# Performance work log

Hardware: AMD Instinct MI355X
Metric: run time of the kernel (lower is better)

The kernel has to match this reference:

```python
import jax, jax.numpy as jnp
import numpy as np

NUM_GROUPS = 32
EPS = 1e-6

def group_norm(x, gamma, beta):
    b, c, h, w = x.shape
    xg = x.reshape(b, NUM_GROUPS, c // NUM_GROUPS, h, w)
    mean = xg.mean(axis=(2, 3, 4), keepdims=True)
    var = xg.var(axis=(2, 3, 4), keepdims=True)
    xg = (xg - mean) * jax.lax.rsqrt(var + EPS)
    x = xg.reshape(b, c, h, w)
    return x * gamma[None, :, None, None] + beta[None, :, None, None]

def conv1x1(x, w, b):
    # x: [B,C,H,W], w: [Cout,Cin], b: [Cout]
    return jnp.einsum('bchw,oc->bohw', x, w) + b[None, :, None, None]

def setup_inputs() -> dict:
    key = jax.random.key(0)
    ks = jax.random.split(key, 11)
    B, C, H, W = 4, 512, 64, 64
    s = 1.0 / np.sqrt(C)
    return {
        'x': jax.random.normal(ks[0], (B, C, H, W), dtype=jnp.float32),
        'gn_gamma': jnp.ones((C,), jnp.float32),
        'gn_beta': jnp.zeros((C,), jnp.float32),
        'wq': jax.random.normal(ks[1], (C, C), jnp.float32) * s,
        'bq': jnp.zeros((C,), jnp.float32),
        'wk': jax.random.normal(ks[2], (C, C), jnp.float32) * s,
        'bk': jnp.zeros((C,), jnp.float32),
        'wv': jax.random.normal(ks[3], (C, C), jnp.float32) * s,
        'bv': jnp.zeros((C,), jnp.float32),
        'wo': jax.random.normal(ks[4], (C, C), jnp.float32) * s,
        'bo': jnp.zeros((C,), jnp.float32),
    }

def reference(x, gn_gamma, gn_beta, wq, bq, wk, bk, wv, bv, wo, bo):
    b, c, H, W = x.shape
    h = group_norm(x, gn_gamma, gn_beta)
    q = conv1x1(h, wq, bq).reshape(b, c, H * W).transpose(0, 2, 1)  # [B, HW, C]
    k = conv1x1(h, wk, bk).reshape(b, c, H * W)                      # [B, C, HW]
    v = conv1x1(h, wv, bv).reshape(b, c, H * W).transpose(0, 2, 1)  # [B, HW, C]
    attn = jnp.einsum('bnc,bcm->bnm', q, k) * (c ** -0.5)            # [B, HW, HW]
    attn = jax.nn.softmax(attn, axis=-1)
    out = jnp.einsum('bnm,bmc->bnc', attn, v)                        # [B, HW, C]
    out = out.transpose(0, 2, 1).reshape(b, c, H, W)
    return x + conv1x1(out, wo, bo)
```

## Files before the change

### kernel.cpp

```cpp
#include <hip/hip_runtime.h>
#include <cstdint>
#include <cstddef>

typedef __attribute__((ext_vector_type(8))) short short8;
typedef __attribute__((ext_vector_type(8))) _Float16 half8;
typedef __attribute__((ext_vector_type(4))) float f32x4;
typedef __attribute__((ext_vector_type(16))) float f32x16;

#define C_ 512
#define S_ 4096
#define B_ 4
#define EPS_ 1e-6f
#define SCALE_ 0.04419417382415922f

__device__ __forceinline__ ushort f2bf(float f) {
    union { float f; uint32_t u; } v; v.f = f;
    uint32_t r = v.u + 0x7FFFu + ((v.u >> 16) & 1u);
    return (ushort)(r >> 16);
}

__global__ void wconv_kernel(const float* __restrict__ wq, const float* __restrict__ wk,
                             const float* __restrict__ wv, const float* __restrict__ wo,
                             ushort* __restrict__ out) {
    int i = blockIdx.x * 256 + threadIdx.x;
    out[i]          = f2bf(wq[i]);
    out[262144 + i] = f2bf(wk[i]);
    out[524288 + i] = f2bf(wv[i]);
    out[786432 + i] = f2bf(wo[i]);
}

__global__ __launch_bounds__(512) void gn_stats_kernel(const float* __restrict__ x,
                                                       float* __restrict__ stats) {
    int bg = blockIdx.x;
    const float* xp = x + (size_t)bg * 16 * S_;
    float sum = 0.f, ss = 0.f;
    for (int i = threadIdx.x; i < 16 * S_; i += 512) {
        float v = xp[i];
        sum += v; ss += v * v;
    }
    #pragma unroll
    for (int off = 32; off; off >>= 1) {
        sum += __shfl_down(sum, off);
        ss  += __shfl_down(ss, off);
    }
    __shared__ float r0[8], r1[8];
    int wid = threadIdx.x >> 6;
    if ((threadIdx.x & 63) == 0) { r0[wid] = sum; r1[wid] = ss; }
    __syncthreads();
    if (threadIdx.x == 0) {
        float ts = 0.f, tq = 0.f;
        #pragma unroll
        for (int w = 0; w < 8; w++) { ts += r0[w]; tq += r1[w]; }
        float mean = ts / 65536.f;
        float var  = tq / 65536.f - mean * mean;
        stats[bg * 2]     = mean;
        stats[bg * 2 + 1] = rsqrtf(var + EPS_);
    }
}

__global__ __launch_bounds__(256) void gn_apply_kernel(const float* __restrict__ x,
        const float* __restrict__ gamma, const float* __restrict__ beta,
        const float* __restrict__ stats, ushort* __restrict__ h_t) {
    int sc = blockIdx.x, g = blockIdx.y, b = blockIdx.z;
    int c0 = g * 16;
    int bg = b * 32 + g;
    float mean = stats[bg * 2], rstd = stats[bg * 2 + 1];
    int t = threadIdx.x;
    __shared__ float tile[16][257];
    const float* xp = x + ((size_t)b * C_ + c0) * S_ + sc * 256;
    {
        int c = t >> 4, s0 = (t & 15) * 4;
        const float* src = xp + (size_t)c * S_;
        #pragma unroll
        for (int j = 0; j < 4; j++) {
            float4 d = *(const float4*)(src + s0 + 64 * j);
            tile[c][s0 + 64 * j + 0] = d.x;
            tile[c][s0 + 64 * j + 1] = d.y;
            tile[c][s0 + 64 * j + 2] = d.z;
            tile[c][s0 + 64 * j + 3] = d.w;
        }
    }
    __syncthreads();
    {
        float vv[16];
        #pragma unroll
        for (int ci = 0; ci < 16; ci++) {
            float a = rstd * gamma[c0 + ci];
            float bb2 = beta[c0 + ci] - mean * a;
            vv[ci] = tile[ci][t] * a + bb2;
        }
        uint4 lo, hi;
        lo.x = (uint32_t)f2bf(vv[0])  | ((uint32_t)f2bf(vv[1])  << 16);
        lo.y = (uint32_t)f2bf(vv[2])  | ((uint32_t)f2bf(vv[3])  << 16);
        lo.z = (uint32_t)f2bf(vv[4])  | ((uint32_t)f2bf(vv[5])  << 16);
        lo.w = (uint32_t)f2bf(vv[6])  | ((uint32_t)f2bf(vv[7])  << 16);
        hi.x = (uint32_t)f2bf(vv[8])  | ((uint32_t)f2bf(vv[9])  << 16);
        hi.y = (uint32_t)f2bf(vv[10]) | ((uint32_t)f2bf(vv[11]) << 16);
        hi.z = (uint32_t)f2bf(vv[12]) | ((uint32_t)f2bf(vv[13]) << 16);
        hi.w = (uint32_t)f2bf(vv[14]) | ((uint32_t)f2bf(vv[15]) << 16);
        ushort* dst = h_t + ((size_t)b * S_ + sc * 256 + t) * C_ + c0;
        *(uint4*)dst = lo;
        *(uint4*)(dst + 8) = hi;
    }
}

template <int MODE>
__global__ __launch_bounds__(256, 2) void gemm_kernel(
        const ushort* __restrict__ A,
        const ushort* __restrict__ Bt,
        const float* __restrict__ bias,
        void* __restrict__ outp,
        const float* __restrict__ xres,
        float scale) {
    int bb = blockIdx.z;
    int m0 = blockIdx.y * 64;
    int n0 = blockIdx.x * 128;
    const ushort* Bp = Bt + (size_t)bb * S_ * C_ + (size_t)n0 * C_;
    __shared__ ushort Al[64 * 64];
    __shared__ ushort Bl[128 * 64];
    int t = threadIdx.x, lane = t & 63, wid = t >> 6;
    int wm = (wid >> 1) * 32, wn = (wid & 1) * 64;
    f32x4 acc[2][4] = {};
    for (int k0 = 0; k0 < 512; k0 += 64) {
        #pragma unroll
        for (int i = 0; i < 2; i++) {
            int cid = t + i * 256;
            int row = cid >> 3, cc = cid & 7;
            uint4 d = *(const uint4*)(A + (size_t)(m0 + row) * 512 + k0 + cc * 8);
            *(uint4*)((char*)Al + row * 128 + ((cc * 16) ^ ((row & 7) << 4))) = d;
        }
        #pragma unroll
        for (int i = 0; i < 4; i++) {
            int cid = t + i * 256;
            int row = cid >> 3, cc = cid & 7;
            uint4 d = *(const uint4*)(Bp + (size_t)row * 512 + k0 + cc * 8);
            *(uint4*)((char*)Bl + row * 128 + ((cc * 16) ^ ((row & 7) << 4))) = d;
        }
        __syncthreads();
        #pragma unroll
        for (int ks = 0; ks < 2; ks++) {
            short8 af[2], bfrag[4];
            #pragma unroll
            for (int i = 0; i < 2; i++) {
                int row = wm + i * 16 + (lane & 15);
                af[i] = *(const short8*)((char*)Al + row * 128 + ((ks * 64 + (lane >> 4) * 16) ^ ((row & 7) << 4)));
            }
            #pragma unroll
            for (int j = 0; j < 4; j++) {
                int row = wn + j * 16 + (lane & 15);
                bfrag[j] = *(const short8*)((char*)Bl + row * 128 + ((ks * 64 + (lane >> 4) * 16) ^ ((row & 7) << 4)));
            }
            #pragma unroll
            for (int i = 0; i < 2; i++)
                #pragma unroll
                for (int j = 0; j < 4; j++)
                    acc[i][j] = __builtin_amdgcn_mfma_f32_16x16x32_bf16(af[i], bfrag[j], acc[i][j], 0, 0, 0);
        }
        __syncthreads();
    }
    int rr = (lane >> 4) * 4;
    #pragma unroll
    for (int i = 0; i < 2; i++) {
        int mb = m0 + wm + i * 16 + rr;
        float bs[4];
        #pragma unroll
        for (int r = 0; r < 4; r++) bs[r] = bias[mb + r];
        #pragma unroll
        for (int j = 0; j < 4; j++) {
            int n = n0 + wn + j * 16 + (lane & 15);
            if (MODE == 0) {
                ushort* O = (ushort*)outp + (size_t)bb * S_ * C_ + (size_t)n * C_ + mb;
                uint2 pp;
                pp.x = (uint32_t)f2bf((acc[i][j][0] + bs[0]) * scale) |
                       ((uint32_t)f2bf((acc[i][j][1] + bs[1]) * scale) << 16);
                pp.y = (uint32_t)f2bf((acc[i][j][2] + bs[2]) * scale) |
                       ((uint32_t)f2bf((acc[i][j][3] + bs[3]) * scale) << 16);
                *(uint2*)O = pp;
            } else if (MODE == 1) {
                ushort* O = (ushort*)outp + (size_t)bb * C_ * S_ + (size_t)mb * S_ + n;
                #pragma unroll
                for (int r = 0; r < 4; r++) O[(size_t)r * S_] = f2bf(acc[i][j][r] + bs[r]);
            } else {
                float* O = (float*)outp + (size_t)bb * C_ * S_ + (size_t)mb * S_ + n;
                const float* X = xres + (size_t)bb * C_ * S_ + (size_t)mb * S_ + n;
                #pragma unroll
                for (int r = 0; r < 4; r++) O[(size_t)r * S_] = X[(size_t)r * S_] + acc[i][j][r] + bs[r];
            }
        }
    }
}

#define KBUF_SZ  65536
#define SLDS_OFF 131072
#define PLDS_OFF 149504
#define STM_OFF  158720

__device__ __forceinline__ void stage_k(const ushort* kp, int kv0, int wid, int lane, char* Kbuf) {
    #pragma unroll
    for (int p = 0; p < 8; p++) {
        int row = wid * 8 + p;
        const char* src = (const char*)(kp + (size_t)(kv0 + row) * C_) + ((lane * 16) ^ ((row & 7) << 4));
        __builtin_amdgcn_global_load_lds(
            (const __attribute__((address_space(1))) unsigned int*)src,
            (__attribute__((address_space(3))) unsigned int*)(Kbuf + row * 1024),
            16, 0, 0);
    }
}

__global__ __launch_bounds__(512, 2) void attn_kernel(const ushort* __restrict__ q_t,
        const ushort* __restrict__ k_t, const ushort* __restrict__ v,
        ushort* __restrict__ ao_t) {
    constexpr int NIT = S_ / 64;
    int qb = blockIdx.x, bb = blockIdx.y;
    int s0 = qb * 64;
    const ushort* qp = q_t + (size_t)bb * S_ * C_;
    const ushort* kp = k_t + (size_t)bb * S_ * C_;
    const ushort* vp = v   + (size_t)bb * C_ * S_;

    extern __shared__ char lds[];
    char* Kbuf0 = lds;
    char* Kbuf1 = lds + KBUF_SZ;
    _Float16* S_lds = (_Float16*)(lds + SLDS_OFF);
    char*  P_lds = lds + PLDS_OFF;
    float* st_m  = (float*)(lds + STM_OFF);
    float* st_l  = st_m + 64;
    float* st_f  = st_m + 128;

    int t = threadIdx.x, lane = t & 63, wid = t >> 6;
    int l31 = lane & 31, lh = lane >> 5;
    int qt = (wid >> 2) & 1, nt = (wid >> 1) & 1, ch = wid & 1;

    if (t < 64) { st_m[t] = -1e30f; st_l[t] = 0.f; }

    short8 qf[16];
    {
        const ushort* qrow = qp + (size_t)(s0 + qt * 32 + l31) * C_ + ch * 256 + lh * 8;
        #pragma unroll
        for (int ks = 0; ks < 16; ks++)
            qf[ks] = *(const short8*)(qrow + ks * 16);
    }
    f32x16 o_[2][2] = {};

    stage_k(kp, 0, wid, lane, Kbuf0);
    asm volatile("s_waitcnt vmcnt(0) lgkmcnt(0)" ::: "memory");
    __builtin_amdgcn_s_barrier();
    asm volatile("" ::: "memory");

    for (int it = 0; it < NIT; it++) {
        int kv0 = it * 64;
        char* Kcur = (it & 1) ? Kbuf1 : Kbuf0;
        char* Knxt = (it & 1) ? Kbuf0 : Kbuf1;

        short8 vb[2][4];
        {
            const ushort* vdb = vp + (size_t)(wid * 64 + l31) * S_ + kv0 + lh * 8;
            #pragma unroll
            for (int dt = 0; dt < 2; dt++)
                #pragma unroll
                for (int ks2 = 0; ks2 < 4; ks2++)
                    vb[dt][ks2] = *(const short8*)(vdb + (size_t)dt * 32 * S_ + ks2 * 16);
        }
        if (it + 1 < NIT)
            stage_k(kp, kv0 + 64, wid, lane, Knxt);

        f32x16 sacc = {};
        {
            int krow = nt * 32 + l31;
            const char* kb = Kcur + krow * 1024;
            int sw = (krow & 7) << 4;
            int cb0 = ch * 512 + lh * 16;
            #pragma unroll
            for (int ks = 0; ks < 16; ks++) {
                short8 kf = *(const short8*)(kb + ((cb0 + ks * 32) ^ sw));
                sacc = __builtin_amdgcn_mfma_f32_32x32x16_bf16(qf[ks], kf, sacc, 0, 0, 0);
            }
        }
        {
            _Float16* Sp = S_lds + (size_t)ch * 4608 + (size_t)(qt * 32) * 72 + nt * 32 + l31;
            #pragma unroll
            for (int r = 0; r < 16; r++) {
                int qrow = (r & 3) + 8 * (r >> 2) + 4 * lh;
                Sp[qrow * 72] = (_Float16)sacc[r];
            }
        }
        asm volatile("s_waitcnt lgkmcnt(0)" ::: "memory");
        __builtin_amdgcn_s_barrier();
        asm volatile("" ::: "memory");

        {
            int row = t >> 3, j = t & 7;
            half8 h0 = *(const half8*)((const char*)S_lds + (size_t)row * 144 + j * 16);
            half8 h1 = *(const half8*)((const char*)S_lds + 9216 + (size_t)row * 144 + j * 16);
            float sv[8];
            #pragma unroll
            for (int i = 0; i < 8; i++) sv[i] = (float)h0[i] + (float)h1[i];
            float mx = sv[0];
            #pragma unroll
            for (int i = 1; i < 8; i++) mx = fmaxf(mx, sv[i]);
            mx = fmaxf(mx, __shfl_xor(mx, 1));
            mx = fmaxf(mx, __shfl_xor(mx, 2));
            mx = fmaxf(mx, __shfl_xor(mx, 4));
            float mold = st_m[row];
            float mnew = fmaxf(mold, mx);
            float ps = 0.f;
            uint32_t pk[4];
            #pragma unroll
            for (int i = 0; i < 4; i++) {
                float p0 = __expf(sv[2 * i]     - mnew);
                float p1 = __expf(sv[2 * i + 1] - mnew);
                ps += p0 + p1;
                pk[i] = (uint32_t)f2bf(p0) | ((uint32_t)f2bf(p1) << 16);
            }
            *(uint4*)(P_lds + (size_t)row * 144 + j * 16) = *(uint4*)pk;
            ps += __shfl_xor(ps, 1); ps += __shfl_xor(ps, 2); ps += __shfl_xor(ps, 4);
            float f = __expf(mold - mnew);
            if (j == 0) {
                st_m[row] = mnew;
                st_l[row] = st_l[row] * f + ps;
                st_f[row] = f;
            }
        }
        asm volatile("s_waitcnt lgkmcnt(0)" ::: "memory");
        __builtin_amdgcn_s_barrier();
        asm volatile("" ::: "memory");

        {
            #pragma unroll
            for (int qt2 = 0; qt2 < 2; qt2++) {
                f32x4 f0 = *(const f32x4*)(st_f + qt2 * 32 + 0  + 4 * lh);
                f32x4 f1 = *(const f32x4*)(st_f + qt2 * 32 + 8  + 4 * lh);
                f32x4 f2 = *(const f32x4*)(st_f + qt2 * 32 + 16 + 4 * lh);
                f32x4 f3 = *(const f32x4*)(st_f + qt2 * 32 + 24 + 4 * lh);
                float fr[16];
                #pragma unroll
                for (int e = 0; e < 4; e++) {
                    fr[e] = f0[e]; fr[4 + e] = f1[e]; fr[8 + e] = f2[e]; fr[12 + e] = f3[e];
                }
                #pragma unroll
                for (int dt = 0; dt < 2; dt++)
                    #pragma unroll
                    for (int r = 0; r < 16; r++)
                        o_[qt2][dt][r] *= fr[r];
            }
            short8 pa[2][4];
            #pragma unroll
            for (int qt2 = 0; qt2 < 2; qt2++)
                #pragma unroll
                for (int ks2 = 0; ks2 < 4; ks2++)
                    pa[qt2][ks2] = *(const short8*)(P_lds + (size_t)(qt2 * 32 + l31) * 144 + ks2 * 32 + lh * 16);
            #pragma unroll
            for (int qt2 = 0; qt2 < 2; qt2++)
                #pragma unroll
                for (int dt = 0; dt < 2; dt++)
                    #pragma unroll
                    for (int ks2 = 0; ks2 < 4; ks2++)
                        o_[qt2][dt] = __builtin_amdgcn_mfma_f32_32x32x16_bf16(pa[qt2][ks2], vb[dt][ks2], o_[qt2][dt], 0, 0, 0);
        }
        asm volatile("s_waitcnt vmcnt(0) lgkmcnt(0)" ::: "memory");
        __builtin_amdgcn_s_barrier();
        asm volatile("" ::: "memory");
    }

    #pragma unroll
    for (int qt2 = 0; qt2 < 2; qt2++) {
        f32x4 l0 = *(const f32x4*)(st_l + qt2 * 32 + 0  + 4 * lh);
        f32x4 l1 = *(const f32x4*)(st_l + qt2 * 32 + 8  + 4 * lh);
        f32x4 l2 = *(const f32x4*)(st_l + qt2 * 32 + 16 + 4 * lh);
        f32x4 l3 = *(const f32x4*)(st_l + qt2 * 32 + 24 + 4 * lh);
        float rl[16];
        #pragma unroll
        for (int e = 0; e < 4; e++) {
            rl[e] = 1.0f / l0[e]; rl[4 + e] = 1.0f / l1[e];
            rl[8 + e] = 1.0f / l2[e]; rl[12 + e] = 1.0f / l3[e];
        }
        #pragma unroll
        for (int dt = 0; dt < 2; dt++) {
            int d = wid * 64 + dt * 32 + l31;
            #pragma unroll
            for (int r = 0; r < 16; r++) {
                int q = qt2 * 32 + (r & 3) + 8 * (r >> 2) + 4 * lh;
                ao_t[((size_t)bb * S_ + s0 + q) * C_ + d] = f2bf(o_[qt2][dt][r] * rl[r]);
            }
        }
    }
}

extern "C" void kernel_launch(void* const* d_in, const int* in_sizes, int n_in,
                              void* d_out, int out_size, void* d_ws, size_t ws_size,
                              hipStream_t stream) {
    const float* x  = (const float*)d_in[0];
    const float* gg = (const float*)d_in[1];
    const float* gb = (const float*)d_in[2];
    const float* wq = (const float*)d_in[3];
    const float* bq = (const float*)d_in[4];
    const float* wk = (const float*)d_in[5];
    const float* bk = (const float*)d_in[6];
    const float* wv = (const float*)d_in[7];
    const float* bv = (const float*)d_in[8];
    const float* wo = (const float*)d_in[9];
    const float* bo = (const float*)d_in[10];
    float* out = (float*)d_out;

    char* ws = (char*)d_ws;
    const size_t BUF = (size_t)B_ * S_ * C_ * 2;
    ushort* h_t  = (ushort*)(ws);
    ushort* q_t  = (ushort*)(ws + BUF);
    ushort* k_t  = (ushort*)(ws + 2 * BUF);
    ushort* v_n  = (ushort*)(ws + 3 * BUF);
    ushort* ao_t = (ushort*)(ws + 4 * BUF);
    ushort* wb   = (ushort*)(ws + 5 * BUF);
    float* stats = (float*)(ws + 5 * BUF + 4 * 524288);

    wconv_kernel<<<1024, 256, 0, stream>>>(wq, wk, wv, wo, wb);
    gn_stats_kernel<<<128, 512, 0, stream>>>(x, stats);
    gn_apply_kernel<<<dim3(16, 32, B_), 256, 0, stream>>>(x, gg, gb, stats, h_t);

    dim3 ggrid(32, 8, B_);
    gemm_kernel<0><<<ggrid, 256, 0, stream>>>(wb,          h_t, bq, (void*)q_t, nullptr, SCALE_);
    gemm_kernel<0><<<ggrid, 256, 0, stream>>>(wb + 262144, h_t, bk, (void*)k_t, nullptr, 1.0f);
    gemm_kernel<1><<<ggrid, 256, 0, stream>>>(wb + 524288, h_t, bv, (void*)v_n, nullptr, 1.0f);

    attn_kernel<<<dim3(64, B_), 512, 159488, stream>>>(q_t, k_t, v_n, ao_t);

    gemm_kernel<2><<<ggrid, 256, 0, stream>>>(wb + 786432, ao_t, bo, (void*)out, x, 1.0f);
}
```

Before: 467.4 us.

## Enlarge GEMM tiles with async LDS double-buffering and lazy softmax rescale in attention

The projection GEMM moves to 128x128 tiles using 32x32x16 MFMA, with double-buffered LDS filled by global_load_lds, so one barrier per k-step overlaps loads with compute. The attention kernel remaps block IDs to a 1D grid that interleaves batches and query blocks, and hoists the V base pointer. It also adds a lazy online-softmax rescale: the running max is updated only when it grows by more than a threshold, and a shared flag skips the output rescale multiply otherwise. The lazy rescale assumes exponent headroom and adds an extra LDS flag with its reset.

```diff
diff --git a/kernel.cpp b/kernel.cpp
--- a/kernel.cpp
+++ b/kernel.cpp
@@ -113,78 +113,104 @@
         const float* __restrict__ xres,
         float scale) {
     int bb = blockIdx.z;
-    int m0 = blockIdx.y * 64;
+    int m0 = blockIdx.y * 128;
     int n0 = blockIdx.x * 128;
-    const ushort* Bp = Bt + (size_t)bb * S_ * C_ + (size_t)n0 * C_;
-    __shared__ ushort Al[64 * 64];
-    __shared__ ushort Bl[128 * 64];
+    const ushort* Ap = A + (size_t)m0 * 512;
+    const ushort* Bp = Bt + (size_t)bb * S_ * C_ + (size_t)n0 * 512;
+
+    extern __shared__ char lds[];
+
     int t = threadIdx.x, lane = t & 63, wid = t >> 6;
-    int wm = (wid >> 1) * 32, wn = (wid & 1) * 64;
-    f32x4 acc[2][4] = {};
+    int l31 = lane & 31, lh = lane >> 5;
+    int wm = (wid >> 1) * 64, wn = (wid & 1) * 64;
+
+    f32x16 acc[2][2] = {};
+
+    #define G_STAGE(sbuf, k0)                                                            \
+        {                                                                                \
+            char* Adst = lds + (sbuf) * 16384;                                           \
+            char* Bdst = lds + 32768 + (sbuf) * 16384;                                   \
+            _Pragma("unroll")                                                            \
+            for (int i_ = 0; i_ < 4; i_++) {                                             \
+                int cb = wid * 64 + i_ * 256;                                            \
+                int cid = cb + lane;                                                     \
+                int row = cid >> 3, c16 = cid & 7;                                       \
+                int sw = ((c16 * 16) ^ ((row & 7) << 4));                                \
+                const char* sa = (const char*)(Ap + (size_t)row * 512 + (k0)) + sw;      \
+                __builtin_amdgcn_global_load_lds(                                        \
+                    (const __attribute__((address_space(1))) unsigned int*)sa,           \
+                    (__attribute__((address_space(3))) unsigned int*)(Adst + cb * 16),   \
+                    16, 0, 0);                                                           \
+                const char* sb = (const char*)(Bp + (size_t)row * 512 + (k0)) + sw;      \
+                __builtin_amdgcn_global_load_lds(                                        \
+                    (const __attribute__((address_space(1))) unsigned int*)sb,           \
+                    (__attribute__((address_space(3))) unsigned int*)(Bdst + cb * 16),   \
+                    16, 0, 0);                                                           \
+            }                                                                            \
+        }
+
+    G_STAGE(0, 0);
+    asm volatile("s_waitcnt vmcnt(0)" ::: "memory");
+    __builtin_amdgcn_s_barrier();
+    asm volatile("" ::: "memory");
+
     for (int k0 = 0; k0 < 512; k0 += 64) {
-        #pragma unroll
-        for (int i = 0; i < 2; i++) {
-            int cid = t + i * 256;
-            int row = cid >> 3, cc = cid & 7;
-            uint4 d = *(const uint4*)(A + (size_t)(m0 + row) * 512 + k0 + cc * 8);
-            *(uint4*)((char*)Al + row * 128 + ((cc * 16) ^ ((row & 7) << 4))) = d;
-        }
-        #pragma unroll
-        for (int i = 0; i < 4; i++) {
-            int cid = t + i * 256;
-            int row = cid >> 3, cc = cid & 7;
-            uint4 d = *(const uint4*)(Bp + (size_t)row * 512 + k0 + cc * 8);
-            *(uint4*)((char*)Bl + row * 128 + ((cc * 16) ^ ((row & 7) << 4))) = d;
-        }
-        __syncthreads();
-        #pragma unroll
-        for (int ks = 0; ks < 2; ks++) {
-            short8 af[2], bfrag[4];
+        int s = (k0 >> 6) & 1;
+        if (k0 + 64 < 512) G_STAGE(s ^ 1, k0 + 64);
+        char* Al = lds + s * 16384;
+        char* Bl = lds + 32768 + s * 16384;
+        #pragma unroll
+        for (int ks = 0; ks < 4; ks++) {
+            short8 af[2], bfr[2];
             #pragma unroll
             for (int i = 0; i < 2; i++) {
-                int row = wm + i * 16 + (lane & 15);
-                af[i] = *(const short8*)((char*)Al + row * 128 + ((ks * 64 + (lane >> 4) * 16) ^ ((row & 7) << 4)));
-            }
-            #pragma unroll
-            for (int j = 0; j < 4; j++) {
-                int row = wn + j * 16 + (lane & 15);
-                bfrag[j] = *(const short8*)((char*)Bl + row * 128 + ((ks * 64 + (lane >> 4) * 16) ^ ((row & 7) << 4)));
+                int rowa = wm + i * 32 + l31;
+                af[i] = *(const short8*)(Al + rowa * 128 + ((ks * 32 + lh * 16) ^ ((rowa & 7) << 4)));
+                int rowb = wn + i * 32 + l31;
+                bfr[i] = *(const short8*)(Bl + rowb * 128 + ((ks * 32 + lh * 16) ^ ((rowb & 7) << 4)));
             }
             #pragma unroll
             for (int i = 0; i < 2; i++)
                 #pragma unroll
-                for (int j = 0; j < 4; j++)
-                    acc[i][j] = __builtin_amdgcn_mfma_f32_16x16x32_bf16(af[i], bfrag[j], acc[i][j], 0, 0, 0);
-        }
-        __syncthreads();
-    }
-    int rr = (lane >> 4) * 4;
+                for (int j = 0; j < 2; j++)
+                    acc[i][j] = __builtin_amdgcn_mfma_f32_32x32x16_bf16(af[i], bfr[j], acc[i][j], 0, 0, 0);
+        }
+        asm volatile("s_waitcnt vmcnt(0) lgkmcnt(0)" ::: "memory");
+        __builtin_amdgcn_s_barrier();
+        asm volatile("" ::: "memory");
+    }
+    #undef G_STAGE
+
     #pragma unroll
     for (int i = 0; i < 2; i++) {
-        int mb = m0 + wm + i * 16 + rr;
-        float bs[4];
-        #pragma unroll
-        for (int r = 0; r < 4; r++) bs[r] = bias[mb + r];
-        #pragma unroll
-        for (int j = 0; j < 4; j++) {
-            int n = n0 + wn + j * 16 + (lane & 15);
-            if (MODE == 0) {
-                ushort* O = (ushort*)outp + (size_t)bb * S_ * C_ + (size_t)n * C_ + mb;
-                uint2 pp;
-                pp.x = (uint32_t)f2bf((acc[i][j][0] + bs[0]) * scale) |
-                       ((uint32_t)f2bf((acc[i][j][1] + bs[1]) * scale) << 16);
-                pp.y = (uint32_t)f2bf((acc[i][j][2] + bs[2]) * scale) |
-                       ((uint32_t)f2bf((acc[i][j][3] + bs[3]) * scale) << 16);
-                *(uint2*)O = pp;
-            } else if (MODE == 1) {
-                ushort* O = (ushort*)outp + (size_t)bb * C_ * S_ + (size_t)mb * S_ + n;
-                #pragma unroll
-                for (int r = 0; r < 4; r++) O[(size_t)r * S_] = f2bf(acc[i][j][r] + bs[r]);
-            } else {
-                float* O = (float*)outp + (size_t)bb * C_ * S_ + (size_t)mb * S_ + n;
-                const float* X = xres + (size_t)bb * C_ * S_ + (size_t)mb * S_ + n;
-                #pragma unroll
-                for (int r = 0; r < 4; r++) O[(size_t)r * S_] = X[(size_t)r * S_] + acc[i][j][r] + bs[r];
+        #pragma unroll
+        for (int q = 0; q < 4; q++) {
+            int mbase = m0 + wm + i * 32 + q * 8 + 4 * lh;
+            float bs[4];
+            #pragma unroll
+            for (int r = 0; r < 4; r++) bs[r] = bias[mbase + r];
+            #pragma unroll
+            for (int j = 0; j < 2; j++) {
+                int n = n0 + wn + j * 32 + l31;
+                if (MODE == 0) {
+                    ushort* O = (ushort*)outp + ((size_t)bb * S_ + n) * C_ + mbase;
+                    uint2 pp;
+                    pp.x = (uint32_t)f2bf((acc[i][j][q * 4 + 0] + bs[0]) * scale) |
+                           ((uint32_t)f2bf((acc[i][j][q * 4 + 1] + bs[1]) * scale) << 16);
+                    pp.y = (uint32_t)f2bf((acc[i][j][q * 4 + 2] + bs[2]) * scale) |
+                           ((uint32_t)f2bf((acc[i][j][q * 4 + 3] + bs[3]) * scale) << 16);
+                    *(uint2*)O = pp;
+                } else if (MODE == 1) {
+                    ushort* O = (ushort*)outp + (size_t)bb * C_ * S_ + (size_t)mbase * S_ + n;
+                    #pragma unroll
+                    for (int r = 0; r < 4; r++) O[(size_t)r * S_] = f2bf(acc[i][j][q * 4 + r] + bs[r]);
+                } else {
+                    float* O = (float*)outp + (size_t)bb * C_ * S_ + (size_t)mbase * S_ + n;
+                    const float* X = xres + (size_t)bb * C_ * S_ + (size_t)mbase * S_ + n;
+                    #pragma unroll
+                    for (int r = 0; r < 4; r++)
+                        O[(size_t)r * S_] = X[(size_t)r * S_] + acc[i][j][q * 4 + r] + bs[r];
+                }
             }
         }
     }
@@ -211,7 +237,9 @@
         const ushort* __restrict__ k_t, const ushort* __restrict__ v,
         ushort* __restrict__ ao_t) {
     constexpr int NIT = S_ / 64;
-    int qb = blockIdx.x, bb = blockIdx.y;
+    int id = blockIdx.x;
+    int bb = (id & 7) >> 1;
+    int qb = ((id & 1) << 5) | (id >> 3);
     int s0 = qb * 64;
     const ushort* qp = q_t + (size_t)bb * S_ * C_;
     const ushort* kp = k_t + (size_t)bb * S_ * C_;
@@ -225,12 +253,14 @@
     float* st_m  = (float*)(lds + STM_OFF);
     float* st_l  = st_m + 64;
     float* st_f  = st_m + 128;
+    int*   rflag = (int*)(st_m + 192);
 
     int t = threadIdx.x, lane = t & 63, wid = t >> 6;
     int l31 = lane & 31, lh = lane >> 5;
     int qt = (wid >> 2) & 1, nt = (wid >> 1) & 1, ch = wid & 1;
 
     if (t < 64) { st_m[t] = -1e30f; st_l[t] = 0.f; }
+    if (t == 0) *rflag = 0;
 
     short8 qf[16];
     {
@@ -240,6 +270,8 @@
             qf[ks] = *(const short8*)(qrow + ks * 16);
     }
     f32x16 o_[2][2] = {};
+
+    const ushort* vdb_base = vp + (size_t)(wid * 64 + l31) * S_ + lh * 8;
 
     stage_k(kp, 0, wid, lane, Kbuf0);
     asm volatile("s_waitcnt vmcnt(0) lgkmcnt(0)" ::: "memory");
@@ -253,7 +285,7 @@
 
         short8 vb[2][4];
         {
-            const ushort* vdb = vp + (size_t)(wid * 64 + l31) * S_ + kv0 + lh * 8;
+            const ushort* vdb = vdb_base + kv0;
             #pragma unroll
             for (int dt = 0; dt < 2; dt++)
                 #pragma unroll
@@ -301,7 +333,9 @@
             mx = fmaxf(mx, __shfl_xor(mx, 2));
             mx = fmaxf(mx, __shfl_xor(mx, 4));
             float mold = st_m[row];
-            float mnew = fmaxf(mold, mx);
+            bool need = (mx > mold + 6.0f);
+            float mnew = need ? mx : mold;
+            if (need) *rflag = 1;
             float ps = 0.f;
             uint32_t pk[4];
             #pragma unroll
@@ -313,11 +347,11 @@
             }
             *(uint4*)(P_lds + (size_t)row * 144 + j * 16) = *(uint4*)pk;
             ps += __shfl_xor(ps, 1); ps += __shfl_xor(ps, 2); ps += __shfl_xor(ps, 4);
-            float f = __expf(mold - mnew);
             if (j == 0) {
-                st_m[row] = mnew;
-                st_l[row] = st_l[row] * f + ps;
-                st_f[row] = f;
+                float ef = need ? __expf(mold - mnew) : 1.0f;
+                if (need) st_m[row] = mnew;
+                st_f[row] = ef;
+                st_l[row] = st_l[row] * ef + ps;
             }
         }
         asm volatile("s_waitcnt lgkmcnt(0)" ::: "memory");
@@ -325,22 +359,24 @@
         asm volatile("" ::: "memory");
 
         {
-            #pragma unroll
-            for (int qt2 = 0; qt2 < 2; qt2++) {
-                f32x4 f0 = *(const f32x4*)(st_f + qt2 * 32 + 0  + 4 * lh);
-                f32x4 f1 = *(const f32x4*)(st_f + qt2 * 32 + 8  + 4 * lh);
-                f32x4 f2 = *(const f32x4*)(st_f + qt2 * 32 + 16 + 4 * lh);
-                f32x4 f3 = *(const f32x4*)(st_f + qt2 * 32 + 24 + 4 * lh);
-                float fr[16];
+            if (*rflag) {
                 #pragma unroll
-                for (int e = 0; e < 4; e++) {
-                    fr[e] = f0[e]; fr[4 + e] = f1[e]; fr[8 + e] = f2[e]; fr[12 + e] = f3[e];
+                for (int qt2 = 0; qt2 < 2; qt2++) {
+                    f32x4 f0 = *(const f32x4*)(st_f + qt2 * 32 + 0  + 4 * lh);
+                    f32x4 f1 = *(const f32x4*)(st_f + qt2 * 32 + 8  + 4 * lh);
+                    f32x4 f2 = *(const f32x4*)(st_f + qt2 * 32 + 16 + 4 * lh);
+                    f32x4 f3 = *(const f32x4*)(st_f + qt2 * 32 + 24 + 4 * lh);
+                    float fr[16];
+                    #pragma unroll
+                    for (int e = 0; e < 4; e++) {
+                        fr[e] = f0[e]; fr[4 + e] = f1[e]; fr[8 + e] = f2[e]; fr[12 + e] = f3[e];
+                    }
+                    #pragma unroll
+                    for (int dt = 0; dt < 2; dt++)
+                        #pragma unroll
+                        for (int r = 0; r < 16; r++)
+                            o_[qt2][dt][r] *= fr[r];
                 }
-                #pragma unroll
-                for (int dt = 0; dt < 2; dt++)
-                    #pragma unroll
-                    for (int r = 0; r < 16; r++)
-                        o_[qt2][dt][r] *= fr[r];
             }
             short8 pa[2][4];
             #pragma unroll
@@ -359,6 +395,7 @@
         asm volatile("s_waitcnt vmcnt(0) lgkmcnt(0)" ::: "memory");
         __builtin_amdgcn_s_barrier();
         asm volatile("" ::: "memory");
+        if (t == 0) *rflag = 0;
     }
 
     #pragma unroll
@@ -415,12 +452,12 @@
     gn_stats_kernel<<<128, 512, 0, stream>>>(x, stats);
     gn_apply_kernel<<<dim3(16, 32, B_), 256, 0, stream>>>(x, gg, gb, stats, h_t);
 
-    dim3 ggrid(32, 8, B_);
-    gemm_kernel<0><<<ggrid, 256, 0, stream>>>(wb,          h_t, bq, (void*)q_t, nullptr, SCALE_);
-    gemm_kernel<0><<<ggrid, 256, 0, stream>>>(wb + 262144, h_t, bk, (void*)k_t, nullptr, 1.0f);
-    gemm_kernel<1><<<ggrid, 256, 0, stream>>>(wb + 524288, h_t, bv, (void*)v_n, nullptr, 1.0f);
-
-    attn_kernel<<<dim3(64, B_), 512, 159488, stream>>>(q_t, k_t, v_n, ao_t);
-
-    gemm_kernel<2><<<ggrid, 256, 0, stream>>>(wb + 786432, ao_t, bo, (void*)out, x, 1.0f);
-}
+    dim3 ggrid(32, 4, B_);
+    gemm_kernel<0><<<ggrid, 256, 65536, stream>>>(wb,          h_t, bq, (void*)q_t, nullptr, SCALE_);
+    gemm_kernel<0><<<ggrid, 256, 65536, stream>>>(wb + 262144, h_t, bk, (void*)k_t, nullptr, 1.0f);
+    gemm_kernel<1><<<ggrid, 256, 65536, stream>>>(wb + 524288, h_t, bv, (void*)v_n, nullptr, 1.0f);
+
+    attn_kernel<<<256, 512, 159552, stream>>>(q_t, k_t, v_n, ao_t);
+
+    gemm_kernel<2><<<ggrid, 256, 65536, stream>>>(wb + 786432, ao_t, bo, (void*)out, x, 1.0f);
+}
```

Measured after the change: 450.2 us. 3.7% less time.
